# Kernel optimization log

Measured on AMD Instinct MI355X. Metric: run time of the kernel, lower is better.

## Reference

```python
import jax, jax.numpy as jnp
import numpy as np


def _l2norm(x, axis):
    return x / jnp.maximum(jnp.linalg.norm(x, axis=axis, keepdims=True), 1e-12)


def setup_inputs() -> dict:
    key = jax.random.key(0)
    ks = jax.random.split(key, 16)
    N, D, F, TI, HD = 1000, 100, 100, 512, 128
    # binary doc-word membership masks, ~50 words per document
    masks = (jax.random.uniform(ks[0], (D, N)) < 0.05).astype(jnp.float32)
    # sparse symmetric normalized word-graph adjacency
    a = (jax.random.uniform(ks[1], (N, N)) < 0.01).astype(jnp.float32)
    adj = jnp.maximum(a, a.T) + jnp.eye(N, dtype=jnp.float32)
    dinv = 1.0 / jnp.sqrt(adj.sum(axis=1))
    train_adj = adj * dinv[:, None] * dinv[None, :]
    bows_vec = jax.random.normal(ks[2], (N, F), dtype=jnp.float32) * 0.1
    image_features = jax.random.normal(ks[3], (D, TI), dtype=jnp.float32)

    def sc(i, sh):
        return jax.random.normal(ks[i], sh, dtype=jnp.float32) * np.float32(1.0 / np.sqrt(sh[0]))

    return {
        'epoch': 3, 'epochs': 10,
        'train_adj': train_adj, 'masks': masks, 'bows_vec': bows_vec,
        'image_features': image_features,
        'W_g1': sc(4, (F, F)), 'W_g2': sc(5, (F, F)),
        'W_h1': sc(6, (F, F)), 'b_h1': jnp.zeros(F, jnp.float32),
        'W_h2': sc(7, (F, F)), 'b_h2': jnp.zeros(F, jnp.float32),
        'W_mu2': sc(8, (F, 1)), 'b_mu2': jnp.zeros(1, jnp.float32),
        'W_eta2': sc(9, (F, 1)), 'b_eta2': jnp.zeros(1, jnp.float32),
        'W_gamma2': sc(10, (F, 1)), 'b_gamma2': jnp.zeros(1, jnp.float32),
        'w_m': sc(11, (F, 1)), 'W_beta': sc(12, (F, 1)),
        'W_m1': sc(13, (TI, HD)), 'b_m1': jnp.zeros(HD, jnp.float32),
        'W_m2': sc(14, (HD, 1)), 'b_m2': jnp.zeros(1, jnp.float32),
    }


def reference(epoch, epochs, train_adj, masks, bows_vec, image_features,
              W_g1, W_g2, W_h1, b_h1, W_h2, b_h2,
              W_mu2, b_mu2, W_eta2, b_eta2, W_gamma2, b_gamma2,
              w_m, W_beta, W_m1, b_m1, W_m2, b_m2):
    N = train_adj.shape[0]
    # --- GcnNet: 2-layer GCN over word graph; doc embedding = masked mean pool ---
    H1 = jax.nn.relu(train_adj @ (bows_vec @ W_g1))        # [N,100]
    H = train_adj @ (H1 @ W_g2)                            # [N,100]
    cnt = masks.sum(axis=1, keepdims=True)                 # [D,1]
    H_p = (masks @ H) / jnp.maximum(cnt, 1.0)              # [D,100]

    H_eli = jax.nn.relu(jax.nn.relu(H @ W_h1 + b_h1) @ W_h2 + b_h2)
    H_eli_norm = _l2norm(H_eli, axis=1)                    # [N,100]

    mu = jax.nn.relu(H_p @ W_mu2 + b_mu2)                  # [D,1]
    # dropout disabled (eval mode)
    eta = jax.nn.relu(H_p @ W_eta2 + b_eta2)               # [D,1]
    gamma = jax.nn.relu(H_p @ W_gamma2 + b_gamma2)         # [D,1]

    sparsity = (epoch / epochs) * 0.3                      # python float (static)
    flat = w_m.reshape(-1)
    j = int(round(sparsity * flat.shape[0]))
    order = jnp.argsort(flat)                              # ascending; drop lowest j
    binary = jnp.zeros_like(flat).at[order[j:]].set(1.0)
    mask_ste = flat + jax.lax.stop_gradient(binary - flat) # forward==binary
    w_pruned = mask_ste.reshape(-1, 1) * W_beta            # [100,1]
    beta_ = _l2norm((H @ w_pruned)[:, 0], axis=0)          # [N]
    beta = masks @ beta_[:, None]                          # [D,1]

    Z_ = jax.nn.relu(H_eli_norm @ H_eli_norm.T)            # [N,N]

    # per-doc sum over distinct word pairs of h_i . h_j ; ||h||=1 so
    # sum_{a<b} h_a.h_b = (||sum_a h_a||^2 - k)/2 with k = #words in doc
    s = masks @ H_eli_norm                                 # [D,100]
    k = masks.sum(axis=1)                                  # [D]
    Z = jax.nn.relu(0.5 * (jnp.sum(s * s, axis=1) - k))[:, None]  # [D,1]

    # Z_event: per-doc [N,N] with entries at local positions p,q < k_i (p!=q)
    # (original indexes Z_ with LOCAL sorted positions 0..k_i-1; kept faithful)
    pos = jnp.arange(N)
    valid = (pos[None, :] < k[:, None]).astype(jnp.float32)       # [D,N]
    E = jnp.exp(-jnp.square(2.0 - 2.0 * Z_)) * (1.0 - jnp.eye(N)) # [N,N]
    Z_event = E[None, :, :] * valid[:, :, None] * valid[:, None, :]  # [D,N,N]

    lambda_texts = jax.nn.sigmoid(mu + beta + eta * jnp.exp(-gamma * Z))
    h_img = jax.nn.relu(image_features @ W_m1 + b_m1)
    lambda_imgs = h_img @ W_m2 + b_m2                      # MLP(512,128,1)
    lambda_total = jax.nn.sigmoid(lambda_texts + lambda_imgs)
    return (lambda_total, Z_, beta_, gamma, eta, Z_event, H)
```

## Files before the change

### kernel.cpp

```cpp
#include <hip/hip_runtime.h>
#include <hip/hip_bf16.h>

typedef __hip_bfloat16 bf;

#define NN   1000
#define DD   100
#define FF   100
#define TIF  512
#define HDD  128
#define EB   256
#define ACAP 96
#define MCAP 192

#define O_LAM 0
#define O_Z   100
#define O_B3  1000100
#define O_GAM 1001100
#define O_ETA 1001200
#define O_ZE  1001300
#define O_H   101001300

#define ZTOT 25000000L

__device__ __forceinline__ float ldf(const void* p, int i, int F32){
  return F32 ? ((const float*)p)[i] : __bfloat162float(((const __hip_bfloat16*)p)[i]);
}

__device__ __forceinline__ float blk_red(float v, volatile float* red, int tid){
#pragma unroll
  for (int o=32;o>0;o>>=1) v += __shfl_down(v,o,64);
  if ((tid&63)==0) red[tid>>6]=v;
  __syncthreads();
  float r = red[0]+red[1];
  __syncthreads();
  return r;
}

__device__ __forceinline__ int sniffF32(const unsigned short* __restrict__ p, int tid){
  int lane = tid & 63;
  const ushort4* q = (const ushort4*)p;
  ushort4 a = q[lane*2], b = q[lane*2+1];
  int c = 0;
  c += (((a.x>>7)&0xFF)>=0xE0); c += (((a.y>>7)&0xFF)>=0xE0);
  c += (((a.z>>7)&0xFF)>=0xE0); c += (((a.w>>7)&0xFF)>=0xE0);
  c += (((b.x>>7)&0xFF)>=0xE0); c += (((b.y>>7)&0xFF)>=0xE0);
  c += (((b.z>>7)&0xFF)>=0xE0); c += (((b.w>>7)&0xFF)>=0xE0);
#pragma unroll
  for (int o=32;o>0;o>>=1) c += __shfl_xor(c,o,64);
  return c > 8;
}

__device__ __forceinline__ void zero_span(uint4* __restrict__ zb, long off, long cnt,
                                          int zi, int nzb, int tid, int bdim){
  long per = (cnt + nzb - 1)/nzb;
  long s = (long)zi*per; if (s>cnt) s=cnt;
  long e = s+per; if (e>cnt) e=cnt;
  uint4 z; z.x=z.y=z.z=z.w=0u;
  for (long i=off+s+tid; i<off+e; i+=bdim) zb[i]=z;
}

__global__ void k_build(const void* __restrict__ A, const void* __restrict__ masks,
                        const void* __restrict__ wm, const void* __restrict__ Wbeta,
                        const void* __restrict__ img, const void* __restrict__ Wm1,
                        const void* __restrict__ bm1, const void* __restrict__ Wm2,
                        const void* __restrict__ bm2,
                        const unsigned short* __restrict__ Xu16,
                        const int* epoch, const int* epochs,
                        int* a_idx, float* a_val, int* a_nnz,
                        int* m_idx, int* m_cnt, float* wpr, float* sumsq,
                        float* limg, int* flag, uint4* __restrict__ zb){
  int b = blockIdx.x; int lane = threadIdx.x;
  if (b >= NN+DD+1+DD){ zero_span(zb, 0L, 5500000L, b-(NN+DD+1+DD), 1024, lane, 64); return; }
  int F32 = sniffF32(Xu16, lane);
  if (b < NN){
    int i=b, nn=0;
    for (int base=0;base<NN;base+=64){
      int c=base+lane; float v=0.f;
      if (c<NN) v=ldf(A, i*NN+c, F32);
      unsigned long long m=__ballot(v!=0.f);
      if (v!=0.f){
        int pos=nn+__popcll(m&((1ull<<lane)-1ull));
        if (pos<ACAP){ a_idx[i*ACAP+pos]=c; a_val[i*ACAP+pos]=v; }
      }
      nn+=__popcll(m);
    }
    if (lane==0) a_nnz[i]=min(nn,ACAP);
  } else if (b < NN+DD){
    int d=b-NN, nn=0;
    for (int base=0;base<NN;base+=64){
      int c=base+lane; float v=0.f;
      if (c<NN) v=ldf(masks, d*NN+c, F32);
      unsigned long long m=__ballot(v!=0.f);
      if (v!=0.f){
        int pos=nn+__popcll(m&((1ull<<lane)-1ull));
        if (pos<MCAP) m_idx[d*MCAP+pos]=c;
      }
      nn+=__popcll(m);
    }
    if (lane==0) m_cnt[d]=min(nn,MCAP);
  } else if (b == NN+DD){
    __shared__ float w[FF];
    for (int t=lane;t<FF;t+=64) w[t]=ldf(wm, t, F32);
    __syncthreads();
    float sp = 0.3f*(float)epoch[0]/(float)epochs[0];
    int j=(int)lroundf(sp*(float)FF);
    for (int t=lane;t<FF;t+=64){
      float v=w[t]; int r=0;
      for (int u=0;u<FF;u++){ float vu=w[u]; r += ((vu<v)||(vu==v && u<t)) ? 1 : 0; }
      wpr[t] = (r>=j)? ldf(Wbeta, t, F32) : 0.f;
    }
    if (lane==0){ sumsq[0]=0.f; flag[0]=F32; }
  } else {
    int d = b - (NN+DD+1);
    __shared__ float ir[TIF];
    for (int t=lane;t<TIF;t+=64) ir[t]=ldf(img, d*TIF+t, F32);
    __syncthreads();
    float acc=0.f;
    for (int h=lane; h<HDD; h+=64){
      float a=ldf(bm1, h, F32);
#pragma unroll 4
      for (int t=0;t<TIF;t++) a=fmaf(ir[t], ldf(Wm1, t*HDD+h, F32), a);
      acc = fmaf(fmaxf(a,0.f), ldf(Wm2, h, F32), acc);
    }
#pragma unroll
    for (int o=32;o>0;o>>=1) acc += __shfl_down(acc,o,64);
    if (lane==0) limg[d]=acc+ldf(bm2,0,F32);
  }
}

template<bool WSRC>
__global__ void k_mm100(const void* __restrict__ Asrc, const void* __restrict__ W,
                        const int* flag, float* __restrict__ C,
                        uint4* __restrict__ zb, long zoff){
  int row=blockIdx.x, tx=threadIdx.x;
  if (row >= NN){ zero_span(zb, zoff, 2000000L, row-NN, 512, tx, 128); return; }
  int F32 = flag[0];
  __shared__ float ar[FF];
  if (WSRC){ const float* Af=(const float*)Asrc; for(int t=tx;t<FF;t+=128) ar[t]=Af[row*FF+t]; }
  else     { for(int t=tx;t<FF;t+=128) ar[t]=ldf(Asrc, row*FF+t, F32); }
  __syncthreads();
  if (tx<FF){
    float a=0.f;
#pragma unroll 4
    for (int c=0;c<FF;c++) a=fmaf(ar[c], ldf(W, c*FF+tx, F32), a);
    C[row*FF+tx]=a;
  }
}

__global__ void k_spmm(const float* __restrict__ B, const int* __restrict__ a_idx,
                       const float* __restrict__ a_val, const int* __restrict__ a_nnz,
                       float* __restrict__ C, float* __restrict__ outb, int relu,
                       uint4* __restrict__ zb, long zoff){
  int row=blockIdx.x, tx=threadIdx.x;
  if (row >= NN){ zero_span(zb, zoff, 2000000L, row-NN, 512, tx, 128); return; }
  __shared__ int sidx[ACAP]; __shared__ float sval[ACAP];
  int nn=a_nnz[row];
  for (int t=tx;t<nn;t+=128){ sidx[t]=a_idx[row*ACAP+t]; sval[t]=a_val[row*ACAP+t]; }
  __syncthreads();
  if (tx<FF){
    float a=0.f;
    for (int m=0;m<nn;m++) a=fmaf(sval[m], B[sidx[m]*FF+tx], a);
    if (relu) a=fmaxf(a,0.f);
    C[row*FF+tx]=a;
    if (outb) outb[row*FF+tx]=a;
  }
}

__global__ void k_rowchain(const float* __restrict__ Hh,
                           const void* __restrict__ Wh1, const void* __restrict__ bh1,
                           const void* __restrict__ Wh2, const void* __restrict__ bh2,
                           const float* __restrict__ wpr, const int* flag,
                           float* __restrict__ Hn, float* __restrict__ HnT,
                           float* __restrict__ hw, float* sumsq,
                           uint4* __restrict__ zb){
  int i=blockIdx.x, tx=threadIdx.x;
  if (i >= NN){ zero_span(zb, 13500000L, 4000000L, i-NN, 1024, tx, 128); return; }
  int F32 = flag[0];
  __shared__ float hr[FF], t1[FF];
  __shared__ float red[2];
  for (int t=tx;t<FF;t+=128) hr[t]=Hh[i*FF+t];
  __syncthreads();
  if (tx<FF){
    float a=ldf(bh1, tx, F32);
#pragma unroll 4
    for (int c=0;c<FF;c++) a=fmaf(hr[c], ldf(Wh1, c*FF+tx, F32), a);
    t1[tx]=fmaxf(a,0.f);
  }
  __syncthreads();
  float hel=0.f;
  if (tx<FF){
    float s=ldf(bh2, tx, F32);
#pragma unroll 4
    for (int c=0;c<FF;c++) s=fmaf(t1[c], ldf(Wh2, c*FF+tx, F32), s);
    hel=fmaxf(s,0.f);
  }
  float phw = (tx<FF)? hr[tx]*wpr[tx] : 0.f;
  float rs2 = blk_red(hel*hel, red, tx);
  float rhw = blk_red(phw, red, tx);
  float rinv = 1.f/fmaxf(sqrtf(rs2), 1e-12f);
  if (tx<FF){ float v=hel*rinv; Hn[i*FF+tx]=v; HnT[tx*NN+i]=v; }
  if (tx==0){ hw[i]=rhw; atomicAdd(sumsq, rhw*rhw); }
}

__global__ void k_doc(const float* __restrict__ Hh, const float* __restrict__ Hn,
                      const float* __restrict__ hw, const float* __restrict__ sumsq,
                      const int* __restrict__ m_idx, const int* __restrict__ m_cnt,
                      const void* Wmu, const void* bmu, const void* Weta, const void* beta_b,
                      const void* Wgam, const void* bgam, const int* flag,
                      const float* __restrict__ limg,
                      int* v_k, float* __restrict__ out, uint4* __restrict__ zb){
  int d=blockIdx.x, tx=threadIdx.x;
  if (d >= DD+8){ zero_span(zb, 17500000L, 1500000L, d-(DD+8), 384, tx, 128); return; }
  if (d >= DD){
    int i=(d-DD)*128+tx;
    if (i<NN){
      float rinv=1.f/fmaxf(sqrtf(sumsq[0]),1e-12f);
      out[O_B3+i]=hw[i]*rinv;
    }
    return;
  }
  int F32 = flag[0];
  __shared__ int sidx[MCAP]; __shared__ float red[2];
  int cnt=m_cnt[d];
  for (int t=tx;t<cnt;t+=128) sidx[t]=m_idx[d*MCAP+t];
  __syncthreads();
  float accH=0.f, accS=0.f;
  if (tx<FF) for (int m=0;m<cnt;m++){ int n=sidx[m]; accH+=Hh[n*FF+tx]; accS+=Hn[n*FF+tx]; }
  float Hp = accH/fmaxf((float)cnt,1.f);
  float pmu = (tx<FF)? Hp*ldf(Wmu, tx, F32)  : 0.f;
  float peta= (tx<FF)? Hp*ldf(Weta, tx, F32) : 0.f;
  float pgam= (tx<FF)? Hp*ldf(Wgam, tx, F32) : 0.f;
  float phw=0.f;
  for (int m=tx;m<cnt;m+=128) phw+=hw[sidx[m]];
  float rmu =blk_red(pmu,red,tx);
  float reta=blk_red(peta,red,tx);
  float rgam=blk_red(pgam,red,tx);
  float rs2 =blk_red(accS*accS,red,tx);
  float rhw =blk_red(phw,red,tx);
  if (tx==0){
    float mu =fmaxf(rmu +ldf(bmu,0,F32),   0.f);
    float eta=fmaxf(reta+ldf(beta_b,0,F32),0.f);
    float gam=fmaxf(rgam+ldf(bgam,0,F32),  0.f);
    float Zd =fmaxf(0.5f*(rs2-(float)cnt), 0.f);
    float beta=rhw/fmaxf(sqrtf(sumsq[0]),1e-12f);
    float lt=1.f/(1.f+expf(-(mu+beta+eta*expf(-gam*Zd))));
    v_k[d]=cnt;
    out[O_LAM+d]=1.f/(1.f+expf(-(lt+limg[d])));
    out[O_GAM+d]=gam;
    out[O_ETA+d]=eta;
  }
}

__global__ __launch_bounds__(256) void k_z(const float* __restrict__ HnT,
                                           float* __restrict__ outZ, float* __restrict__ Eblk,
                                           uint4* __restrict__ zb){
  int b = blockIdx.x;
  int tid=threadIdx.x;
  if (b >= 256){ zero_span(zb, 19000000L, 6000000L, b-256, 1024, tid, 256); return; }
  int bi=(b&15)*64, bj=(b>>4)*64;
  __shared__ float At[FF*68], Bt[FF*68];
  for (int t=tid;t<FF*64;t+=256){
    int k=t>>6, ii=t&63;
    int gi=bi+ii, gj=bj+ii;
    At[k*68+ii] = (gi<NN)? HnT[k*NN+gi] : 0.f;
    Bt[k*68+ii] = (gj<NN)? HnT[k*NN+gj] : 0.f;
  }
  __syncthreads();
  int tx=tid&15, ty=tid>>4;
  float acc[4][4]={};
  for (int k=0;k<FF;k++){
    float4 av=*(float4*)&At[k*68+4*ty];
    float4 bv=*(float4*)&Bt[k*68+4*tx];
    float aa[4]={av.x,av.y,av.z,av.w};
    float bb[4]={bv.x,bv.y,bv.z,bv.w};
#pragma unroll
    for (int q=0;q<4;q++)
#pragma unroll
      for (int r=0;r<4;r++) acc[q][r]=fmaf(aa[q],bb[r],acc[q][r]);
  }
#pragma unroll
  for (int q=0;q<4;q++){
    int gi=bi+4*ty+q; if (gi>=NN) continue;
    float z[4];
#pragma unroll
    for (int r=0;r<4;r++) z[r]=fmaxf(acc[q][r],0.f);
    int gj0=bj+4*tx;
    if (gj0+3<NN){
      float4 zz; zz.x=z[0]; zz.y=z[1]; zz.z=z[2]; zz.w=z[3];
      *(float4*)&outZ[(size_t)gi*NN+gj0]=zz;
    } else {
      for (int r=0;r<4;r++) if (gj0+r<NN) outZ[(size_t)gi*NN+gj0+r]=z[r];
    }
    if (gi<EB && gj0<EB){
#pragma unroll
      for (int r=0;r<4;r++){
        int gj=gj0+r;
        float t2=2.f-2.f*z[r];
        Eblk[gi*EB+gj]=(gi==gj)?0.f:expf(-t2*t2);
      }
    }
  }
}

__global__ void k_fill(const float* __restrict__ Eblk, const int* __restrict__ v_k,
                       float* __restrict__ outZE){
  int d=blockIdx.x; int k=v_k[d]; if (k>EB) k=EB;
  int kk=k*k;
  for (int idx=threadIdx.x; idx<kk; idx+=256){
    int i=idx/k, j=idx-i*k;
    float e=(i==j)?0.f:Eblk[i*EB+j];
    outZE[(size_t)d*1000000 + (size_t)i*1000 + j]=e;
  }
}

extern "C" void kernel_launch(void* const* d_in, const int* in_sizes, int n_in,
                              void* d_out, int out_size, void* d_ws, size_t ws_size,
                              hipStream_t stream) {
  const int* epoch  = (const int*)d_in[0];
  const int* epochs = (const int*)d_in[1];
  const void* A     = d_in[2];
  const void* masks = d_in[3];
  const void* X     = d_in[4];
  const void* img   = d_in[5];
  const void* Wg1   = d_in[6];
  const void* Wg2   = d_in[7];
  const void* Wh1   = d_in[8];
  const void* bh1   = d_in[9];
  const void* Wh2   = d_in[10];
  const void* bh2   = d_in[11];
  const void* Wmu   = d_in[12];
  const void* bmu   = d_in[13];
  const void* Weta  = d_in[14];
  const void* beta_b= d_in[15];
  const void* Wgam  = d_in[16];
  const void* bgam  = d_in[17];
  const void* wm    = d_in[18];
  const void* Wbeta = d_in[19];
  const void* Wm1   = d_in[20];
  const void* bm1   = d_in[21];
  const void* Wm2   = d_in[22];
  const void* bm2   = d_in[23];
  float* out = (float*)d_out;

  float* ws   = (float*)d_ws;
  float* XW   = ws;
  float* H1   = XW  + 100000;
  float* H1W  = H1  + 100000;
  float* Hh   = H1W + 100000;
  float* Hn   = Hh  + 100000;
  float* HnT  = Hn  + 100000;
  float* Eblk = HnT + 100000;
  float* a_val= Eblk+ 65536;
  int* a_idx  = (int*)(a_val + 96000);
  int* a_nnz  = a_idx + 96000;
  int* m_idx  = a_nnz + 1000;
  int* m_cnt  = m_idx + 19200;
  float* wpr  = (float*)(m_cnt + 100);
  float* hw   = wpr + 100;
  float* sumsq= hw + 1000;
  int* v_k    = (int*)(sumsq + 4);
  int* flag   = v_k + 104;
  float* limg = (float*)(flag + 4);

  uint4* zb = (uint4*)((char*)d_out + (size_t)O_ZE*4);

  hipLaunchKernelGGL(k_build, dim3(NN+DD+1+DD+1024), dim3(64), 0, stream,
                     A, masks, wm, Wbeta, img, Wm1, bm1, Wm2, bm2,
                     (const unsigned short*)X, epoch, epochs,
                     a_idx, a_val, a_nnz, m_idx, m_cnt, wpr, sumsq, limg, flag, zb);
  hipLaunchKernelGGL((k_mm100<false>), dim3(NN+512), dim3(128), 0, stream, X, Wg1, flag, XW, zb, 5500000L);
  hipLaunchKernelGGL(k_spmm, dim3(NN+512), dim3(128), 0, stream, XW, a_idx, a_val, a_nnz, H1, (float*)nullptr, 1, zb, 7500000L);
  hipLaunchKernelGGL((k_mm100<true>), dim3(NN+512), dim3(128), 0, stream, (const void*)H1, Wg2, flag, H1W, zb, 9500000L);
  hipLaunchKernelGGL(k_spmm, dim3(NN+512), dim3(128), 0, stream, H1W, a_idx, a_val, a_nnz, Hh, out + O_H, 0, zb, 11500000L);
  hipLaunchKernelGGL(k_rowchain, dim3(NN+1024), dim3(128), 0, stream,
                     Hh, Wh1, bh1, Wh2, bh2, wpr, flag, Hn, HnT, hw, sumsq, zb);
  hipLaunchKernelGGL(k_doc, dim3(DD+8+384), dim3(128), 0, stream,
                     Hh, Hn, hw, sumsq, m_idx, m_cnt,
                     Wmu, bmu, Weta, beta_b, Wgam, bgam, flag, limg, v_k, out, zb);
  hipLaunchKernelGGL(k_z, dim3(256+1024), dim3(256), 0, stream, HnT, out + O_Z, Eblk, zb);
  hipLaunchKernelGGL(k_fill, dim3(DD), dim3(256), 0, stream, Eblk, v_k, out + O_ZE);
}
```

Measured before the change: 694.6 us.

## Fuse nine kernel launches into five and rebalance zero-fill across them

Merges the X@Wg1 matmul into the build kernel, fuses the first spmm with relu and the Wg2 matmul, fuses the second spmm with the row-chain MLP/normalization, and merges the doc-level reductions with the Z_ Gram tile kernel. The large zero-fill of the event tensor is redistributed across the remaining launches. This is meant to cut launch overhead and intermediate global round-trips. The cost is that the fused Wg1 matmul now runs with 64-thread blocks, and the mixed-role blocks in each launch may load-balance unevenly.

```diff
diff --git a/kernel.cpp b/kernel.cpp
--- a/kernel.cpp
+++ b/kernel.cpp
@@ -20,8 +20,6 @@
 #define O_ZE  1001300
 #define O_H   101001300
 
-#define ZTOT 25000000L
-
 __device__ __forceinline__ float ldf(const void* p, int i, int F32){
   return F32 ? ((const float*)p)[i] : __bfloat162float(((const __hip_bfloat16*)p)[i]);
 }
@@ -32,6 +30,15 @@
   if ((tid&63)==0) red[tid>>6]=v;
   __syncthreads();
   float r = red[0]+red[1];
+  __syncthreads();
+  return r;
+}
+__device__ __forceinline__ float blk_red4(float v, volatile float* red, int tid){
+#pragma unroll
+  for (int o=32;o>0;o>>=1) v += __shfl_down(v,o,64);
+  if ((tid&63)==0) red[tid>>6]=v;
+  __syncthreads();
+  float r = red[0]+red[1]+red[2]+red[3];
   __syncthreads();
   return r;
 }
@@ -59,19 +66,20 @@
   for (long i=off+s+tid; i<off+e; i+=bdim) zb[i]=z;
 }
 
-__global__ void k_build(const void* __restrict__ A, const void* __restrict__ masks,
-                        const void* __restrict__ wm, const void* __restrict__ Wbeta,
-                        const void* __restrict__ img, const void* __restrict__ Wm1,
-                        const void* __restrict__ bm1, const void* __restrict__ Wm2,
-                        const void* __restrict__ bm2,
-                        const unsigned short* __restrict__ Xu16,
-                        const int* epoch, const int* epochs,
-                        int* a_idx, float* a_val, int* a_nnz,
-                        int* m_idx, int* m_cnt, float* wpr, float* sumsq,
-                        float* limg, int* flag, uint4* __restrict__ zb){
+__global__ void k1_build(const void* __restrict__ A, const void* __restrict__ masks,
+                         const void* __restrict__ wm, const void* __restrict__ Wbeta,
+                         const void* __restrict__ img, const void* __restrict__ Wm1,
+                         const void* __restrict__ bm1, const void* __restrict__ Wm2,
+                         const void* __restrict__ bm2, const void* __restrict__ X,
+                         const void* __restrict__ Wg1,
+                         const int* epoch, const int* epochs,
+                         int* a_idx, float* a_val, int* a_nnz,
+                         int* m_idx, int* m_cnt, float* wpr, float* sumsq,
+                         float* limg, int* flag, float* __restrict__ XW,
+                         uint4* __restrict__ zb){
   int b = blockIdx.x; int lane = threadIdx.x;
-  if (b >= NN+DD+1+DD){ zero_span(zb, 0L, 5500000L, b-(NN+DD+1+DD), 1024, lane, 64); return; }
-  int F32 = sniffF32(Xu16, lane);
+  if (b >= NN+DD+1+DD+NN){ zero_span(zb, 0L, 8000000L, b-(NN+DD+1+DD+NN), 2048, lane, 64); return; }
+  int F32 = sniffF32((const unsigned short*)X, lane);
   if (b < NN){
     int i=b, nn=0;
     for (int base=0;base<NN;base+=64){
@@ -110,7 +118,7 @@
       wpr[t] = (r>=j)? ldf(Wbeta, t, F32) : 0.f;
     }
     if (lane==0){ sumsq[0]=0.f; flag[0]=F32; }
-  } else {
+  } else if (b < NN+DD+1+DD){
     int d = b - (NN+DD+1);
     __shared__ float ir[TIF];
     for (int t=lane;t<TIF;t+=64) ir[t]=ldf(img, d*TIF+t, F32);
@@ -125,61 +133,68 @@
 #pragma unroll
     for (int o=32;o>0;o>>=1) acc += __shfl_down(acc,o,64);
     if (lane==0) limg[d]=acc+ldf(bm2,0,F32);
-  }
-}
-
-template<bool WSRC>
-__global__ void k_mm100(const void* __restrict__ Asrc, const void* __restrict__ W,
-                        const int* flag, float* __restrict__ C,
-                        uint4* __restrict__ zb, long zoff){
+  } else {
+    int r = b - (NN+DD+1+DD);
+    __shared__ float ar[FF];
+    for (int t=lane;t<FF;t+=64) ar[t]=ldf(X, r*FF+t, F32);
+    __syncthreads();
+    for (int col=lane; col<FF; col+=64){
+      float a=0.f;
+#pragma unroll 4
+      for (int c=0;c<FF;c++) a=fmaf(ar[c], ldf(Wg1, c*FF+col, F32), a);
+      XW[r*FF+col]=a;
+    }
+  }
+}
+
+__global__ void k2_h1(const float* __restrict__ XW, const void* __restrict__ Wg2,
+                      const int* flag, const int* __restrict__ a_idx,
+                      const float* __restrict__ a_val, const int* __restrict__ a_nnz,
+                      float* __restrict__ H1W, uint4* __restrict__ zb){
   int row=blockIdx.x, tx=threadIdx.x;
-  if (row >= NN){ zero_span(zb, zoff, 2000000L, row-NN, 512, tx, 128); return; }
-  int F32 = flag[0];
-  __shared__ float ar[FF];
-  if (WSRC){ const float* Af=(const float*)Asrc; for(int t=tx;t<FF;t+=128) ar[t]=Af[row*FF+t]; }
-  else     { for(int t=tx;t<FF;t+=128) ar[t]=ldf(Asrc, row*FF+t, F32); }
-  __syncthreads();
-  if (tx<FF){
-    float a=0.f;
-#pragma unroll 4
-    for (int c=0;c<FF;c++) a=fmaf(ar[c], ldf(W, c*FF+tx, F32), a);
-    C[row*FF+tx]=a;
-  }
-}
-
-__global__ void k_spmm(const float* __restrict__ B, const int* __restrict__ a_idx,
-                       const float* __restrict__ a_val, const int* __restrict__ a_nnz,
-                       float* __restrict__ C, float* __restrict__ outb, int relu,
-                       uint4* __restrict__ zb, long zoff){
-  int row=blockIdx.x, tx=threadIdx.x;
-  if (row >= NN){ zero_span(zb, zoff, 2000000L, row-NN, 512, tx, 128); return; }
-  __shared__ int sidx[ACAP]; __shared__ float sval[ACAP];
+  if (row >= NN){ zero_span(zb, 8000000L, 5000000L, row-NN, 1280, tx, 128); return; }
+  __shared__ int sidx[ACAP]; __shared__ float sval[ACAP]; __shared__ float t1[FF];
   int nn=a_nnz[row];
   for (int t=tx;t<nn;t+=128){ sidx[t]=a_idx[row*ACAP+t]; sval[t]=a_val[row*ACAP+t]; }
   __syncthreads();
   if (tx<FF){
     float a=0.f;
-    for (int m=0;m<nn;m++) a=fmaf(sval[m], B[sidx[m]*FF+tx], a);
-    if (relu) a=fmaxf(a,0.f);
-    C[row*FF+tx]=a;
-    if (outb) outb[row*FF+tx]=a;
-  }
-}
-
-__global__ void k_rowchain(const float* __restrict__ Hh,
-                           const void* __restrict__ Wh1, const void* __restrict__ bh1,
-                           const void* __restrict__ Wh2, const void* __restrict__ bh2,
-                           const float* __restrict__ wpr, const int* flag,
-                           float* __restrict__ Hn, float* __restrict__ HnT,
-                           float* __restrict__ hw, float* sumsq,
-                           uint4* __restrict__ zb){
+    for (int m=0;m<nn;m++) a=fmaf(sval[m], XW[sidx[m]*FF+tx], a);
+    t1[tx]=fmaxf(a,0.f);
+  }
+  __syncthreads();
+  int F32=flag[0];
+  if (tx<FF){
+    float s=0.f;
+#pragma unroll 4
+    for (int c=0;c<FF;c++) s=fmaf(t1[c], ldf(Wg2, c*FF+tx, F32), s);
+    H1W[row*FF+tx]=s;
+  }
+}
+
+__global__ void k3_h2(const float* __restrict__ H1W, const int* __restrict__ a_idx,
+                      const float* __restrict__ a_val, const int* __restrict__ a_nnz,
+                      const void* __restrict__ Wh1, const void* __restrict__ bh1,
+                      const void* __restrict__ Wh2, const void* __restrict__ bh2,
+                      const float* __restrict__ wpr, const int* flag,
+                      float* __restrict__ Hh, float* __restrict__ Hn,
+                      float* __restrict__ HnT, float* __restrict__ hw, float* sumsq,
+                      float* __restrict__ outH, uint4* __restrict__ zb){
   int i=blockIdx.x, tx=threadIdx.x;
-  if (i >= NN){ zero_span(zb, 13500000L, 4000000L, i-NN, 1024, tx, 128); return; }
-  int F32 = flag[0];
+  if (i >= NN){ zero_span(zb, 13000000L, 5000000L, i-NN, 1280, tx, 128); return; }
+  __shared__ int sidx[ACAP]; __shared__ float sval[ACAP];
   __shared__ float hr[FF], t1[FF];
   __shared__ float red[2];
-  for (int t=tx;t<FF;t+=128) hr[t]=Hh[i*FF+t];
-  __syncthreads();
+  int nn=a_nnz[i];
+  for (int t=tx;t<nn;t+=128){ sidx[t]=a_idx[i*ACAP+t]; sval[t]=a_val[i*ACAP+t]; }
+  __syncthreads();
+  if (tx<FF){
+    float a=0.f;
+    for (int m=0;m<nn;m++) a=fmaf(sval[m], H1W[sidx[m]*FF+tx], a);
+    hr[tx]=a; Hh[i*FF+tx]=a; outH[i*FF+tx]=a;
+  }
+  __syncthreads();
+  int F32=flag[0];
   if (tx<FF){
     float a=ldf(bh1, tx, F32);
 #pragma unroll 4
@@ -202,109 +217,106 @@
   if (tx==0){ hw[i]=rhw; atomicAdd(sumsq, rhw*rhw); }
 }
 
-__global__ void k_doc(const float* __restrict__ Hh, const float* __restrict__ Hn,
+__global__ __launch_bounds__(256) void k4_zdoc(const float* __restrict__ HnT,
+                      const float* __restrict__ Hh, const float* __restrict__ Hn,
                       const float* __restrict__ hw, const float* __restrict__ sumsq,
                       const int* __restrict__ m_idx, const int* __restrict__ m_cnt,
                       const void* Wmu, const void* bmu, const void* Weta, const void* beta_b,
                       const void* Wgam, const void* bgam, const int* flag,
                       const float* __restrict__ limg,
-                      int* v_k, float* __restrict__ out, uint4* __restrict__ zb){
-  int d=blockIdx.x, tx=threadIdx.x;
-  if (d >= DD+8){ zero_span(zb, 17500000L, 1500000L, d-(DD+8), 384, tx, 128); return; }
-  if (d >= DD){
-    int i=(d-DD)*128+tx;
+                      float* __restrict__ out, float* __restrict__ Eblk,
+                      uint4* __restrict__ zb){
+  int b=blockIdx.x, tid=threadIdx.x;
+  if (b >= 360){ zero_span(zb, 18000000L, 7000000L, b-360, 1792, tid, 256); return; }
+  if (b < 256){
+    int bi=(b&15)*64, bj=(b>>4)*64;
+    __shared__ float At[FF*68], Bt[FF*68];
+    for (int t=tid;t<FF*64;t+=256){
+      int k=t>>6, ii=t&63;
+      int gi=bi+ii, gj=bj+ii;
+      At[k*68+ii] = (gi<NN)? HnT[k*NN+gi] : 0.f;
+      Bt[k*68+ii] = (gj<NN)? HnT[k*NN+gj] : 0.f;
+    }
+    __syncthreads();
+    int tx=tid&15, ty=tid>>4;
+    float acc[4][4]={};
+    for (int k=0;k<FF;k++){
+      float4 av=*(float4*)&At[k*68+4*ty];
+      float4 bv=*(float4*)&Bt[k*68+4*tx];
+      float aa[4]={av.x,av.y,av.z,av.w};
+      float bb[4]={bv.x,bv.y,bv.z,bv.w};
+#pragma unroll
+      for (int q=0;q<4;q++)
+#pragma unroll
+        for (int r=0;r<4;r++) acc[q][r]=fmaf(aa[q],bb[r],acc[q][r]);
+    }
+#pragma unroll
+    for (int q=0;q<4;q++){
+      int gi=bi+4*ty+q; if (gi>=NN) continue;
+      float z[4];
+#pragma unroll
+      for (int r=0;r<4;r++) z[r]=fmaxf(acc[q][r],0.f);
+      int gj0=bj+4*tx;
+      if (gj0+3<NN){
+        float4 zz; zz.x=z[0]; zz.y=z[1]; zz.z=z[2]; zz.w=z[3];
+        *(float4*)&out[O_Z+(size_t)gi*NN+gj0]=zz;
+      } else {
+        for (int r=0;r<4;r++) if (gj0+r<NN) out[O_Z+(size_t)gi*NN+gj0+r]=z[r];
+      }
+      if (gi<EB && gj0<EB){
+#pragma unroll
+        for (int r=0;r<4;r++){
+          int gj=gj0+r;
+          float t2=2.f-2.f*z[r];
+          Eblk[gi*EB+gj]=(gi==gj)?0.f:expf(-t2*t2);
+        }
+      }
+    }
+    return;
+  }
+  if (b >= 356){
+    int i=(b-356)*256+tid;
     if (i<NN){
       float rinv=1.f/fmaxf(sqrtf(sumsq[0]),1e-12f);
       out[O_B3+i]=hw[i]*rinv;
     }
     return;
   }
+  int d=b-256;
   int F32 = flag[0];
-  __shared__ int sidx[MCAP]; __shared__ float red[2];
+  __shared__ int sidx[MCAP]; __shared__ float red[4];
   int cnt=m_cnt[d];
-  for (int t=tx;t<cnt;t+=128) sidx[t]=m_idx[d*MCAP+t];
+  for (int t=tid;t<cnt;t+=256) sidx[t]=m_idx[d*MCAP+t];
   __syncthreads();
   float accH=0.f, accS=0.f;
-  if (tx<FF) for (int m=0;m<cnt;m++){ int n=sidx[m]; accH+=Hh[n*FF+tx]; accS+=Hn[n*FF+tx]; }
+  if (tid<FF) for (int m=0;m<cnt;m++){ int n=sidx[m]; accH+=Hh[n*FF+tid]; accS+=Hn[n*FF+tid]; }
   float Hp = accH/fmaxf((float)cnt,1.f);
-  float pmu = (tx<FF)? Hp*ldf(Wmu, tx, F32)  : 0.f;
-  float peta= (tx<FF)? Hp*ldf(Weta, tx, F32) : 0.f;
-  float pgam= (tx<FF)? Hp*ldf(Wgam, tx, F32) : 0.f;
+  float pmu = (tid<FF)? Hp*ldf(Wmu, tid, F32)  : 0.f;
+  float peta= (tid<FF)? Hp*ldf(Weta, tid, F32) : 0.f;
+  float pgam= (tid<FF)? Hp*ldf(Wgam, tid, F32) : 0.f;
   float phw=0.f;
-  for (int m=tx;m<cnt;m+=128) phw+=hw[sidx[m]];
-  float rmu =blk_red(pmu,red,tx);
-  float reta=blk_red(peta,red,tx);
-  float rgam=blk_red(pgam,red,tx);
-  float rs2 =blk_red(accS*accS,red,tx);
-  float rhw =blk_red(phw,red,tx);
-  if (tx==0){
+  for (int m=tid;m<cnt;m+=256) phw+=hw[sidx[m]];
+  float rmu =blk_red4(pmu,red,tid);
+  float reta=blk_red4(peta,red,tid);
+  float rgam=blk_red4(pgam,red,tid);
+  float rs2 =blk_red4(accS*accS,red,tid);
+  float rhw =blk_red4(phw,red,tid);
+  if (tid==0){
     float mu =fmaxf(rmu +ldf(bmu,0,F32),   0.f);
     float eta=fmaxf(reta+ldf(beta_b,0,F32),0.f);
     float gam=fmaxf(rgam+ldf(bgam,0,F32),  0.f);
     float Zd =fmaxf(0.5f*(rs2-(float)cnt), 0.f);
     float beta=rhw/fmaxf(sqrtf(sumsq[0]),1e-12f);
     float lt=1.f/(1.f+expf(-(mu+beta+eta*expf(-gam*Zd))));
-    v_k[d]=cnt;
     out[O_LAM+d]=1.f/(1.f+expf(-(lt+limg[d])));
     out[O_GAM+d]=gam;
     out[O_ETA+d]=eta;
   }
 }
 
-__global__ __launch_bounds__(256) void k_z(const float* __restrict__ HnT,
-                                           float* __restrict__ outZ, float* __restrict__ Eblk,
-                                           uint4* __restrict__ zb){
-  int b = blockIdx.x;
-  int tid=threadIdx.x;
-  if (b >= 256){ zero_span(zb, 19000000L, 6000000L, b-256, 1024, tid, 256); return; }
-  int bi=(b&15)*64, bj=(b>>4)*64;
-  __shared__ float At[FF*68], Bt[FF*68];
-  for (int t=tid;t<FF*64;t+=256){
-    int k=t>>6, ii=t&63;
-    int gi=bi+ii, gj=bj+ii;
-    At[k*68+ii] = (gi<NN)? HnT[k*NN+gi] : 0.f;
-    Bt[k*68+ii] = (gj<NN)? HnT[k*NN+gj] : 0.f;
-  }
-  __syncthreads();
-  int tx=tid&15, ty=tid>>4;
-  float acc[4][4]={};
-  for (int k=0;k<FF;k++){
-    float4 av=*(float4*)&At[k*68+4*ty];
-    float4 bv=*(float4*)&Bt[k*68+4*tx];
-    float aa[4]={av.x,av.y,av.z,av.w};
-    float bb[4]={bv.x,bv.y,bv.z,bv.w};
-#pragma unroll
-    for (int q=0;q<4;q++)
-#pragma unroll
-      for (int r=0;r<4;r++) acc[q][r]=fmaf(aa[q],bb[r],acc[q][r]);
-  }
-#pragma unroll
-  for (int q=0;q<4;q++){
-    int gi=bi+4*ty+q; if (gi>=NN) continue;
-    float z[4];
-#pragma unroll
-    for (int r=0;r<4;r++) z[r]=fmaxf(acc[q][r],0.f);
-    int gj0=bj+4*tx;
-    if (gj0+3<NN){
-      float4 zz; zz.x=z[0]; zz.y=z[1]; zz.z=z[2]; zz.w=z[3];
-      *(float4*)&outZ[(size_t)gi*NN+gj0]=zz;
-    } else {
-      for (int r=0;r<4;r++) if (gj0+r<NN) outZ[(size_t)gi*NN+gj0+r]=z[r];
-    }
-    if (gi<EB && gj0<EB){
-#pragma unroll
-      for (int r=0;r<4;r++){
-        int gj=gj0+r;
-        float t2=2.f-2.f*z[r];
-        Eblk[gi*EB+gj]=(gi==gj)?0.f:expf(-t2*t2);
-      }
-    }
-  }
-}
-
-__global__ void k_fill(const float* __restrict__ Eblk, const int* __restrict__ v_k,
-                       float* __restrict__ outZE){
-  int d=blockIdx.x; int k=v_k[d]; if (k>EB) k=EB;
+__global__ void k5_fill(const float* __restrict__ Eblk, const int* __restrict__ m_cnt,
+                        float* __restrict__ outZE){
+  int d=blockIdx.x; int k=m_cnt[d]; if (k>EB) k=EB;
   int kk=k*k;
   for (int idx=threadIdx.x; idx<kk; idx+=256){
     int i=idx/k, j=idx-i*k;
@@ -344,8 +356,7 @@
 
   float* ws   = (float*)d_ws;
   float* XW   = ws;
-  float* H1   = XW  + 100000;
-  float* H1W  = H1  + 100000;
+  float* H1W  = XW  + 100000;
   float* Hh   = H1W + 100000;
   float* Hn   = Hh  + 100000;
   float* HnT  = Hn  + 100000;
@@ -358,25 +369,23 @@
   float* wpr  = (float*)(m_cnt + 100);
   float* hw   = wpr + 100;
   float* sumsq= hw + 1000;
-  int* v_k    = (int*)(sumsq + 4);
-  int* flag   = v_k + 104;
+  int* flag   = (int*)(sumsq + 4);
   float* limg = (float*)(flag + 4);
 
   uint4* zb = (uint4*)((char*)d_out + (size_t)O_ZE*4);
 
-  hipLaunchKernelGGL(k_build, dim3(NN+DD+1+DD+1024), dim3(64), 0, stream,
-                     A, masks, wm, Wbeta, img, Wm1, bm1, Wm2, bm2,
-                     (const unsigned short*)X, epoch, epochs,
-                     a_idx, a_val, a_nnz, m_idx, m_cnt, wpr, sumsq, limg, flag, zb);
-  hipLaunchKernelGGL((k_mm100<false>), dim3(NN+512), dim3(128), 0, stream, X, Wg1, flag, XW, zb, 5500000L);
-  hipLaunchKernelGGL(k_spmm, dim3(NN+512), dim3(128), 0, stream, XW, a_idx, a_val, a_nnz, H1, (float*)nullptr, 1, zb, 7500000L);
-  hipLaunchKernelGGL((k_mm100<true>), dim3(NN+512), dim3(128), 0, stream, (const void*)H1, Wg2, flag, H1W, zb, 9500000L);
-  hipLaunchKernelGGL(k_spmm, dim3(NN+512), dim3(128), 0, stream, H1W, a_idx, a_val, a_nnz, Hh, out + O_H, 0, zb, 11500000L);
-  hipLaunchKernelGGL(k_rowchain, dim3(NN+1024), dim3(128), 0, stream,
-                     Hh, Wh1, bh1, Wh2, bh2, wpr, flag, Hn, HnT, hw, sumsq, zb);
-  hipLaunchKernelGGL(k_doc, dim3(DD+8+384), dim3(128), 0, stream,
-                     Hh, Hn, hw, sumsq, m_idx, m_cnt,
-                     Wmu, bmu, Weta, beta_b, Wgam, bgam, flag, limg, v_k, out, zb);
-  hipLaunchKernelGGL(k_z, dim3(256+1024), dim3(256), 0, stream, HnT, out + O_Z, Eblk, zb);
-  hipLaunchKernelGGL(k_fill, dim3(DD), dim3(256), 0, stream, Eblk, v_k, out + O_ZE);
-}
+  hipLaunchKernelGGL(k1_build, dim3(NN+DD+1+DD+NN+2048), dim3(64), 0, stream,
+                     A, masks, wm, Wbeta, img, Wm1, bm1, Wm2, bm2, X, Wg1,
+                     epoch, epochs,
+                     a_idx, a_val, a_nnz, m_idx, m_cnt, wpr, sumsq, limg, flag, XW, zb);
+  hipLaunchKernelGGL(k2_h1, dim3(NN+1280), dim3(128), 0, stream,
+                     XW, Wg2, flag, a_idx, a_val, a_nnz, H1W, zb);
+  hipLaunchKernelGGL(k3_h2, dim3(NN+1280), dim3(128), 0, stream,
+                     H1W, a_idx, a_val, a_nnz, Wh1, bh1, Wh2, bh2, wpr, flag,
+                     Hh, Hn, HnT, hw, sumsq, out + O_H, zb);
+  hipLaunchKernelGGL(k4_zdoc, dim3(360+1792), dim3(256), 0, stream,
+                     HnT, Hh, Hn, hw, sumsq, m_idx, m_cnt,
+                     Wmu, bmu, Weta, beta_b, Wgam, bgam, flag, limg,
+                     out, Eblk, zb);
+  hipLaunchKernelGGL(k5_fill, dim3(DD), dim3(256), 0, stream, Eblk, m_cnt, out + O_ZE);
+}
```

Result: faster. 668.7 us (-3.7%).
